# Kernel optimization log

Hardware: AMD Instinct MI355X
Metric: run time of the kernel (lower is better)

Reference implementation:

```python
import jax, jax.numpy as jnp
import numpy as np

NUM_GRAPHS = 64
N, E, H = 100000, 3200000, 64


def _glorot(k, shape):
    fan_in = shape[0]
    return jax.random.normal(k, shape, jnp.float32) * (1.0 / np.sqrt(fan_in))


def setup_inputs() -> dict:
    key = jax.random.key(0)
    ks = jax.random.split(key, 16)
    edge_index = jax.random.randint(ks[0], (2, E), 0, N)
    edge_weight = jax.random.uniform(ks[1], (E,), dtype=jnp.float32)
    batch = jnp.sort(jax.random.randint(ks[2], (N,), 0, NUM_GRAPHS))
    return {
        "edge_index": edge_index,
        "edge_weight": edge_weight,
        "batch": batch,
        "num_nodes": N,
        "W1": _glorot(ks[3], (1, H)), "b1": jnp.zeros((H,), jnp.float32),
        "W2": _glorot(ks[4], (H, H)), "b2": jnp.zeros((H,), jnp.float32),
        "W3": _glorot(ks[5], (H, H)), "b3": jnp.zeros((H,), jnp.float32),
        "W4": _glorot(ks[6], (H, H)), "b4": jnp.zeros((H,), jnp.float32),
        "W5": _glorot(ks[7], (H, H)), "b5": jnp.zeros((H,), jnp.float32),
        "lin_w": _glorot(ks[8], (H, 1)), "lin_b": jnp.zeros((1,), jnp.float32),
    }


def _gcn_layer(x, W, b, src, dst, w, n):
    # GCNConv(normalize=False): linear transform then weighted scatter-add over edges.
    h = x @ W                                  # [N, H]
    m = h[src] * w[:, None]                    # [E, H] messages
    return jax.ops.segment_sum(m, dst, num_segments=n) + b


def reference(edge_index, edge_weight, batch, num_nodes,
              W1, b1, W2, b2, W3, b3, W4, b4, W5, b5, lin_w, lin_b):
    src, dst = edge_index[0], edge_index[1]
    x = jnp.ones((num_nodes, 1), jnp.float32)
    for W, b in ((W1, b1), (W2, b2), (W3, b3), (W4, b4), (W5, b5)):
        x = jax.nn.relu(_gcn_layer(x, W, b, src, dst, edge_weight, num_nodes))
        # dropout p=0.1 is identity in eval mode
    # global mean pool per graph
    sums = jax.ops.segment_sum(x, batch, num_segments=NUM_GRAPHS)      # [G, H]
    counts = jax.ops.segment_sum(jnp.ones((num_nodes,), x.dtype), batch,
                                 num_segments=NUM_GRAPHS)
    pooled = sums / jnp.maximum(counts, 1.0)[:, None]
    return pooled @ lin_w + lin_b                                      # [G, 1]
```

## Files before the change

### kernel.cpp

```cpp
#include <hip/hip_runtime.h>

#define H 64
#define NUM_GRAPHS 64
#define BSHIFT 8
#define BSIZE 256
#define MAXNB 512
#define CHUNK 8192
#define BKT 9216
#define PADE 8
#define CSRB (BKT + BSIZE * PADE)
#define RPB 16

typedef unsigned int uint;
typedef unsigned short ushort;
typedef __attribute__((ext_vector_type(4))) float f32x4;
typedef __attribute__((ext_vector_type(8))) short short8;

__device__ __forceinline__ float bf2f(ushort u) {
    return __uint_as_float(((uint)u) << 16);
}
__device__ __forceinline__ ushort f2bf(float f) {
    uint b = __float_as_uint(f);
    b += 0x7FFFu + ((b >> 16) & 1u);
    return (ushort)(b >> 16);
}

__global__ void init_kernel(int* __restrict__ bucketCur, int NB) {
    int i = blockIdx.x * 256 + threadIdx.x;
    if (i < NB) bucketCur[i] = i * BKT;
}

__global__ __launch_bounds__(1024) void part_kernel(const int* __restrict__ src,
        const int* __restrict__ dst, const float* __restrict__ w,
        int* __restrict__ bucketCur, int2* __restrict__ bucketed, int E, int NB) {
    __shared__ int h[MAXNB];
    __shared__ int basev[MAXNB];
    __shared__ int lbase[MAXNB + 1];
    __shared__ int s[512];
    __shared__ int2 stage[CHUNK];
    int tid = threadIdx.x;
    for (int i = tid; i < NB; i += 1024) h[i] = 0;
    __syncthreads();
    int cbase = blockIdx.x * CHUNK;
    int cend = min(cbase + CHUNK, E);
    for (int e = cbase + tid; e < cend; e += 1024)
        atomicAdd(&h[dst[e] >> BSHIFT], 1);
    __syncthreads();
    for (int i = tid; i < NB; i += 1024) {
        int c = h[i];
        basev[i] = c ? atomicAdd(&bucketCur[i], c) : 0;
    }
    if (tid < 512) s[tid] = (tid < NB) ? h[tid] : 0;
    __syncthreads();
    for (int off = 1; off < 512; off <<= 1) {
        int t = (tid < 512 && tid >= off) ? s[tid - off] : 0;
        __syncthreads();
        if (tid < 512) s[tid] += t;
        __syncthreads();
    }
    if (tid < NB) lbase[tid + 1] = s[tid];
    if (tid == 0) lbase[0] = 0;
    __syncthreads();
    for (int i = tid; i < NB; i += 1024) h[i] = 0;
    __syncthreads();
    for (int e = cbase + tid; e < cend; e += 1024) {
        int d = dst[e];
        int b = d >> BSHIFT;
        int slot = atomicAdd(&h[b], 1);
        stage[lbase[b] + slot] =
            make_int2(((d & (BSIZE - 1)) << 17) | src[e], __float_as_int(w[e]));
    }
    __syncthreads();
    int lane = tid & 63, wv = tid >> 6;
    for (int b = wv; b < NB; b += 16) {
        int lb = lbase[b], cnt = lbase[b + 1] - lb, gb = basev[b];
        int lim = (b + 1) * BKT;
        for (int k = lane; k < cnt; k += 64)
            if (gb + k < lim) bucketed[gb + k] = stage[lb + k];
    }
}

__global__ __launch_bounds__(512) void bsort_kernel(const int* __restrict__ bucketCur,
        const int2* __restrict__ bucketed, uint* __restrict__ csr,
        int2* __restrict__ rowinfo, float* __restrict__ degw, int N) {
    __shared__ int cnt[BSIZE];
    __shared__ int pos[BSIZE];
    __shared__ int cur[BSIZE];
    __shared__ float wsum[BSIZE];
    int b = blockIdx.x;
    int tid = threadIdx.x;
    int nodeBase = b << BSHIFT;
    int nNodes = min(BSIZE, N - nodeBase);
    if (tid < BSIZE) { cnt[tid] = 0; wsum[tid] = 0.f; }
    __syncthreads();
    int ebeg = b * BKT;
    int eend = min(bucketCur[b], ebeg + BKT);
    for (int e = ebeg + tid; e < eend; e += 512)
        atomicAdd(&cnt[bucketed[e].x >> 17], 1);
    __syncthreads();
    int pc = 0;
    if (tid < BSIZE) { pc = (cnt[tid] + PADE - 1) & ~(PADE - 1); pos[tid] = pc; }
    __syncthreads();
    for (int off = 1; off < BSIZE; off <<= 1) {
        int t = (tid < BSIZE && tid >= off) ? pos[tid - off] : 0;
        __syncthreads();
        if (tid < BSIZE) pos[tid] += t;
        __syncthreads();
    }
    int csrBase = b * CSRB;
    if (tid < BSIZE) {
        int excl = pos[tid] - pc;
        cur[tid] = excl;
        if (tid < nNodes) rowinfo[nodeBase + tid] = make_int2(csrBase + excl, cnt[tid]);
    }
    __syncthreads();
    for (int e = ebeg + tid; e < eend; e += 512) {
        int2 v = bucketed[e];
        int dl = v.x >> 17;
        int slot = atomicAdd(&cur[dl], 1);
        uint wb = (uint)v.y;
        wb += 0x7FFFu + ((wb >> 16) & 1u);
        uint w15 = (wb >> 16) & 0x7FFFu;
        csr[csrBase + slot] = (((uint)(v.x & 0x1FFFF)) << 15) | w15;
        atomicAdd(&wsum[dl], __uint_as_float(w15 << 16));
    }
    __syncthreads();
    if (tid < nNodes) degw[nodeBase + tid] = wsum[tid];
}

__global__ void layer1_kernel(const float* __restrict__ degw, const float* __restrict__ W1,
                              const float* __restrict__ b1, ushort* __restrict__ out, int N) {
    int gid = blockIdx.x * 256 + threadIdx.x;
    if (gid >= N * 16) return;
    int i = gid >> 4, c4 = (gid & 15) * 4;
    float d = degw[i];
    uint lo = (uint)f2bf(fmaxf(d * W1[c4 + 0] + b1[c4 + 0], 0.f))
            | ((uint)f2bf(fmaxf(d * W1[c4 + 1] + b1[c4 + 1], 0.f)) << 16);
    uint hi = (uint)f2bf(fmaxf(d * W1[c4 + 2] + b1[c4 + 2], 0.f))
            | ((uint)f2bf(fmaxf(d * W1[c4 + 3] + b1[c4 + 3], 0.f)) << 16);
    *reinterpret_cast<uint2*>(out + ((size_t)i << 6) + c4) = make_uint2(lo, hi);
}

__global__ void count_kernel(const int* __restrict__ batch, float* __restrict__ gcnt, int N) {
    __shared__ int bins[NUM_GRAPHS];
    int tid = threadIdx.x;
    if (tid < NUM_GRAPHS) bins[tid] = 0;
    __syncthreads();
    int node = blockIdx.x * 256 + tid;
    if (node < N) atomicAdd(&bins[batch[node]], 1);
    __syncthreads();
    if (tid < NUM_GRAPHS && bins[tid])
        unsafeAtomicAdd(&gcnt[tid], (float)bins[tid]);
}

template<bool LAST>
__global__ __launch_bounds__(256) void layer_kernel(const int2* __restrict__ rowinfo,
        const uint* __restrict__ csr, const ushort* __restrict__ x,
        const float* __restrict__ W, const float* __restrict__ bvec,
        ushort* __restrict__ out, const int* __restrict__ batch,
        const float* __restrict__ linw, float* __restrict__ gsum, int N) {
    __shared__ alignas(16) ushort Wt[64][72];
    __shared__ alignas(16) ushort AG[RPB][72];
    __shared__ uint pc[4][64];
    __shared__ float gbins[NUM_GRAPHS];
    int tid = threadIdx.x;
    for (int i = tid; i < 64 * 64; i += 256) {
        int k = i >> 6, c = i & 63;
        Wt[c][k] = f2bf(W[i]);
    }
    if (LAST && tid < NUM_GRAPHS) gbins[tid] = 0.f;
    __syncthreads();
    int lane = tid & 63, wid = tid >> 6;
    int hi = lane >> 5;
    const char* xb = (const char*)x + (size_t)((lane & 31) << 2);
    int rowbase = blockIdx.x * RPB;
#pragma unroll 1
    for (int p = 0; p < 4; ++p) {
        int trow = wid * 4 + p;
        int row = rowbase + trow;
        float a0 = 0.f, a1 = 0.f, b0 = 0.f, b1 = 0.f;
        if (row < N) {
            int2 ri = rowinfo[row];
            int beg = ri.x, len = ri.y;
#pragma unroll 1
            for (int ck = 0; ck < len; ck += 64) {
                int idx = ck + lane;
                uint pv = (idx < len) ? __builtin_nontemporal_load(csr + beg + idx) : 0u;
                pc[wid][lane] = pv;
                int grps = (min(64, len - ck) + 7) >> 3;
#pragma unroll
                for (int g = 0; g < 8; ++g) {
                    if (g < grps) {
#pragma unroll
                        for (int jp = 0; jp < 4; ++jp) {
                            uint pp = pc[wid][g * 8 + jp * 2 + hi];
                            uint u = *reinterpret_cast<const uint*>(
                                         xb + ((size_t)(pp >> 15) << 7));
                            float wf = __uint_as_float((pp & 0x7FFFu) << 16);
                            if (g & 1) {
                                b0 = fmaf(wf, __uint_as_float(u << 16), b0);
                                b1 = fmaf(wf, __uint_as_float(u & 0xFFFF0000u), b1);
                            } else {
                                a0 = fmaf(wf, __uint_as_float(u << 16), a0);
                                a1 = fmaf(wf, __uint_as_float(u & 0xFFFF0000u), a1);
                            }
                        }
                    }
                }
            }
        }
        a0 += b0; a1 += b1;
        a0 += __shfl_xor(a0, 32);
        a1 += __shfl_xor(a1, 32);
        if (lane < 32) {
            uint pk = (uint)f2bf(a0) | ((uint)f2bf(a1) << 16);
            *reinterpret_cast<uint*>(&AG[trow][lane << 1]) = pk;
        }
    }
    __syncthreads();
    int cl = lane & 15, kg = lane >> 4;
    int c0 = wid * 16;
    short8 a0v = *reinterpret_cast<const short8*>(&AG[cl][kg * 8]);
    short8 a1v = *reinterpret_cast<const short8*>(&AG[cl][32 + kg * 8]);
    short8 bb0 = *reinterpret_cast<const short8*>(&Wt[c0 + cl][kg * 8]);
    short8 bb1 = *reinterpret_cast<const short8*>(&Wt[c0 + cl][32 + kg * 8]);
    f32x4 acc = {0.f, 0.f, 0.f, 0.f};
    acc = __builtin_amdgcn_mfma_f32_16x16x32_bf16(a0v, bb0, acc, 0, 0, 0);
    acc = __builtin_amdgcn_mfma_f32_16x16x32_bf16(a1v, bb1, acc, 0, 0, 0);
    float bias = bvec[c0 + cl];
    float lw = LAST ? linw[c0 + cl] : 0.f;
#pragma unroll
    for (int j = 0; j < 4; ++j) {
        int r = rowbase + kg * 4 + j;
        if (r < N) {
            float v = fmaxf(acc[j] + bias, 0.f);
            if (!LAST)
                __builtin_nontemporal_store(f2bf(v), out + ((size_t)r << 6) + c0 + cl);
            else
                atomicAdd(&gbins[batch[r]], v * lw);
        }
    }
    if (LAST) {
        __syncthreads();
        if (tid < NUM_GRAPHS) unsafeAtomicAdd(&gsum[tid], gbins[tid]);
    }
}

__global__ void final_kernel(const float* __restrict__ gsum, const float* __restrict__ gcnt,
                             const float* __restrict__ lin_b, float* __restrict__ out) {
    int g = threadIdx.x;
    if (g < NUM_GRAPHS) out[g] = gsum[g] / fmaxf(gcnt[g], 1.f) + lin_b[0];
}

extern "C" void kernel_launch(void* const* d_in, const int* in_sizes, int n_in,
                              void* d_out, int out_size, void* d_ws, size_t ws_size,
                              hipStream_t stream) {
    const int*   edge_index = (const int*)d_in[0];
    const float* ew    = (const float*)d_in[1];
    const int*   batch = (const int*)d_in[2];
    const float* W1    = (const float*)d_in[4];
    const float* b1    = (const float*)d_in[5];
    const float* Wl[4] = {(const float*)d_in[6], (const float*)d_in[8],
                          (const float*)d_in[10], (const float*)d_in[12]};
    const float* bl[4] = {(const float*)d_in[7], (const float*)d_in[9],
                          (const float*)d_in[11], (const float*)d_in[13]};
    const float* linw  = (const float*)d_in[14];
    const float* linb  = (const float*)d_in[15];

    const int E = in_sizes[1];
    const int N = in_sizes[2];
    const int* src = edge_index;
    const int* dst = edge_index + E;
    const int NB = (N + BSIZE - 1) >> BSHIFT;

    char* base = (char*)d_ws;
    size_t featPad = (((size_t)(N + 16) * H * 2) + 255) & ~(size_t)255;
    size_t bktBytes = (((size_t)NB * BKT * 8) + 255) & ~(size_t)255;
    size_t span = 2 * featPad > bktBytes ? 2 * featPad : bktBytes;
    ushort* bufA = (ushort*)base;
    ushort* bufB = (ushort*)(base + featPad);
    int2* bucketed = (int2*)base;
    uint* csr = (uint*)(base + span);
    size_t csrBytes = (((size_t)NB * CSRB * 4) + 255) & ~(size_t)255;
    char* tail = base + span + csrBytes;
    int2* rowinfo   = (int2*)tail;
    int* bucketCur  = (int*)(rowinfo + N);
    float* gsum     = (float*)(bucketCur + MAXNB);
    float* gcnt     = gsum + NUM_GRAPHS;
    float* degw     = gcnt + NUM_GRAPHS;

    const int chunks = (E + CHUNK - 1) / CHUNK;

    init_kernel<<<(NB + 255) / 256, 256, 0, stream>>>(bucketCur, NB);
    hipMemsetAsync(gsum, 0, 2 * NUM_GRAPHS * sizeof(float), stream);
    part_kernel<<<chunks, 1024, 0, stream>>>(src, dst, ew, bucketCur, bucketed, E, NB);
    bsort_kernel<<<NB, 512, 0, stream>>>(bucketCur, bucketed, csr, rowinfo, degw, N);

    layer1_kernel<<<(N * 16 + 255) / 256, 256, 0, stream>>>(degw, W1, b1, bufA, N);
    count_kernel<<<(N + 255) / 256, 256, 0, stream>>>(batch, gcnt, N);

    const int gridL = (N + RPB - 1) / RPB;
    ushort* xin = bufA;
    ushort* xout = bufB;
    for (int l = 0; l < 3; ++l) {
        layer_kernel<false><<<gridL, 256, 0, stream>>>(rowinfo, csr, xin, Wl[l], bl[l],
                xout, batch, linw, gsum, N);
        ushort* t = xin; xin = xout; xout = t;
    }
    layer_kernel<true><<<gridL, 256, 0, stream>>>(rowinfo, csr, xin, Wl[3], bl[3],
            xout, batch, linw, gsum, N);

    final_kernel<<<1, 64, 0, stream>>>(gsum, gcnt, linb, (float*)d_out);
}
```

Baseline: 470.0 us.

## Split GCN layers into column-sliced aggregation and separate MFMA transform kernels

Features are stored as two 32-column bf16 slices instead of row-major 64-wide rows. Each layer is split into an aggregation kernel and a matmul kernel. The aggregation kernel gathers from one slice, with block ids interleaved so neighbouring chunks share a slice. The matmul kernel applies W, bias and ReLU with MFMA over several row tiles per block. The aim is a smaller gather working set per pass so it stays in cache better, at the cost of two launches per layer, an extra round trip of the aggregate through memory, and reading the CSR twice.

```diff
diff --git a/kernel.cpp b/kernel.cpp
--- a/kernel.cpp
+++ b/kernel.cpp
@@ -9,7 +9,6 @@
 #define BKT 9216
 #define PADE 8
 #define CSRB (BKT + BSIZE * PADE)
-#define RPB 16
 
 typedef unsigned int uint;
 typedef unsigned short ushort;
@@ -129,7 +128,7 @@
 }
 
 __global__ void layer1_kernel(const float* __restrict__ degw, const float* __restrict__ W1,
-                              const float* __restrict__ b1, ushort* __restrict__ out, int N) {
+                              const float* __restrict__ b1, ushort* __restrict__ outB, int N) {
     int gid = blockIdx.x * 256 + threadIdx.x;
     if (gid >= N * 16) return;
     int i = gid >> 4, c4 = (gid & 15) * 4;
@@ -138,7 +137,8 @@
             | ((uint)f2bf(fmaxf(d * W1[c4 + 1] + b1[c4 + 1], 0.f)) << 16);
     uint hi = (uint)f2bf(fmaxf(d * W1[c4 + 2] + b1[c4 + 2], 0.f))
             | ((uint)f2bf(fmaxf(d * W1[c4 + 3] + b1[c4 + 3], 0.f)) << 16);
-    *reinterpret_cast<uint2*>(out + ((size_t)i << 6) + c4) = make_uint2(lo, hi);
+    size_t off = (size_t)(c4 >> 5) * N * 32 + ((size_t)i << 5) + (c4 & 31);
+    *reinterpret_cast<uint2*>(outB + off) = make_uint2(lo, hi);
 }
 
 __global__ void count_kernel(const int* __restrict__ batch, float* __restrict__ gcnt, int N) {
@@ -153,15 +153,62 @@
         unsafeAtomicAdd(&gcnt[tid], (float)bins[tid]);
 }
 
-template<bool LAST>
-__global__ __launch_bounds__(256) void layer_kernel(const int2* __restrict__ rowinfo,
-        const uint* __restrict__ csr, const ushort* __restrict__ x,
+__global__ __launch_bounds__(256) void aggA_kernel(const int2* __restrict__ rowinfo,
+        const uint* __restrict__ csr, const ushort* __restrict__ xB,
+        ushort* __restrict__ aggB, int N, int nchunk) {
+    __shared__ uint pc[4][64];
+    int b = blockIdx.x;
+    int r8 = b & 7;
+    int slice = r8 >> 2;
+    int chunk = (b >> 3) * 4 + (r8 & 3);
+    if (chunk >= nchunk) return;
+    int rowbase = chunk * 16;
+    int tid = threadIdx.x, lane = tid & 63, wid = tid >> 6;
+    int hi = lane >> 5;
+    int lch = lane & 31;
+    const char* xsb = (const char*)(xB + (size_t)slice * N * 32) + (lch << 1);
+    ushort* asb = aggB + (size_t)slice * N * 32 + lch;
+    int pcb = hi << 5;
+#pragma unroll 1
+    for (int p = 0; p < 2; ++p) {
+        int row = rowbase + wid * 4 + p * 2 + hi;
+        int rr = min(row, N - 1);
+        int2 ri = rowinfo[rr];
+        int beg = ri.x;
+        int len = (row < N) ? ri.y : 0;
+        int lenm = max(len, __shfl_xor(len, 32));
+        float a0 = 0.f, a1 = 0.f;
+#pragma unroll 1
+        for (int ck = 0; ck < lenm; ck += 32) {
+            int idx = ck + lch;
+            uint pv = (idx < len) ? __builtin_nontemporal_load(csr + beg + idx) : 0u;
+            pc[wid][pcb + lch] = pv;
+            int rem = len - ck;
+#pragma unroll
+            for (int g = 0; g < 4; ++g) {
+                if (g * 8 < rem) {
+#pragma unroll
+                    for (int j = 0; j < 8; ++j) {
+                        uint pp = pc[wid][pcb + g * 8 + j];
+                        float wf = __uint_as_float((pp & 0x7FFFu) << 16);
+                        ushort u = *reinterpret_cast<const ushort*>(
+                                       xsb + ((size_t)(pp >> 15) << 6));
+                        if (g & 1) a1 = fmaf(wf, bf2f(u), a1);
+                        else       a0 = fmaf(wf, bf2f(u), a0);
+                    }
+                }
+            }
+        }
+        if (row < N) asb[(size_t)row << 5] = f2bf(a0 + a1);
+    }
+}
+
+template<bool LAST, int TILES>
+__global__ __launch_bounds__(256) void matB_kernel(const ushort* __restrict__ aggB,
         const float* __restrict__ W, const float* __restrict__ bvec,
-        ushort* __restrict__ out, const int* __restrict__ batch,
+        ushort* __restrict__ outB, const int* __restrict__ batch,
         const float* __restrict__ linw, float* __restrict__ gsum, int N) {
     __shared__ alignas(16) ushort Wt[64][72];
-    __shared__ alignas(16) ushort AG[RPB][72];
-    __shared__ uint pc[4][64];
     __shared__ float gbins[NUM_GRAPHS];
     int tid = threadIdx.x;
     for (int i = tid; i < 64 * 64; i += 256) {
@@ -171,73 +218,34 @@
     if (LAST && tid < NUM_GRAPHS) gbins[tid] = 0.f;
     __syncthreads();
     int lane = tid & 63, wid = tid >> 6;
-    int hi = lane >> 5;
-    const char* xb = (const char*)x + (size_t)((lane & 31) << 2);
-    int rowbase = blockIdx.x * RPB;
-#pragma unroll 1
-    for (int p = 0; p < 4; ++p) {
-        int trow = wid * 4 + p;
-        int row = rowbase + trow;
-        float a0 = 0.f, a1 = 0.f, b0 = 0.f, b1 = 0.f;
-        if (row < N) {
-            int2 ri = rowinfo[row];
-            int beg = ri.x, len = ri.y;
-#pragma unroll 1
-            for (int ck = 0; ck < len; ck += 64) {
-                int idx = ck + lane;
-                uint pv = (idx < len) ? __builtin_nontemporal_load(csr + beg + idx) : 0u;
-                pc[wid][lane] = pv;
-                int grps = (min(64, len - ck) + 7) >> 3;
-#pragma unroll
-                for (int g = 0; g < 8; ++g) {
-                    if (g < grps) {
-#pragma unroll
-                        for (int jp = 0; jp < 4; ++jp) {
-                            uint pp = pc[wid][g * 8 + jp * 2 + hi];
-                            uint u = *reinterpret_cast<const uint*>(
-                                         xb + ((size_t)(pp >> 15) << 7));
-                            float wf = __uint_as_float((pp & 0x7FFFu) << 16);
-                            if (g & 1) {
-                                b0 = fmaf(wf, __uint_as_float(u << 16), b0);
-                                b1 = fmaf(wf, __uint_as_float(u & 0xFFFF0000u), b1);
-                            } else {
-                                a0 = fmaf(wf, __uint_as_float(u << 16), a0);
-                                a1 = fmaf(wf, __uint_as_float(u & 0xFFFF0000u), a1);
-                            }
-                        }
-                    }
-                }
-            }
-        }
-        a0 += b0; a1 += b1;
-        a0 += __shfl_xor(a0, 32);
-        a1 += __shfl_xor(a1, 32);
-        if (lane < 32) {
-            uint pk = (uint)f2bf(a0) | ((uint)f2bf(a1) << 16);
-            *reinterpret_cast<uint*>(&AG[trow][lane << 1]) = pk;
-        }
-    }
-    __syncthreads();
     int cl = lane & 15, kg = lane >> 4;
     int c0 = wid * 16;
-    short8 a0v = *reinterpret_cast<const short8*>(&AG[cl][kg * 8]);
-    short8 a1v = *reinterpret_cast<const short8*>(&AG[cl][32 + kg * 8]);
-    short8 bb0 = *reinterpret_cast<const short8*>(&Wt[c0 + cl][kg * 8]);
-    short8 bb1 = *reinterpret_cast<const short8*>(&Wt[c0 + cl][32 + kg * 8]);
-    f32x4 acc = {0.f, 0.f, 0.f, 0.f};
-    acc = __builtin_amdgcn_mfma_f32_16x16x32_bf16(a0v, bb0, acc, 0, 0, 0);
-    acc = __builtin_amdgcn_mfma_f32_16x16x32_bf16(a1v, bb1, acc, 0, 0, 0);
-    float bias = bvec[c0 + cl];
-    float lw = LAST ? linw[c0 + cl] : 0.f;
+    int cc = c0 + cl;
+    size_t oblk = (size_t)(cc >> 5) * N * 32;
+    for (int t = 0; t < TILES; ++t) {
+        int rowbase = (blockIdx.x * TILES + t) * 16;
+        if (rowbase >= N) break;
+        const ushort* ap0 = aggB + (((size_t)(rowbase + cl)) << 5) + kg * 8;
+        short8 a0v = *reinterpret_cast<const short8*>(ap0);
+        short8 a1v = *reinterpret_cast<const short8*>(ap0 + (size_t)N * 32);
+        short8 bb0 = *reinterpret_cast<const short8*>(&Wt[cc][kg * 8]);
+        short8 bb1 = *reinterpret_cast<const short8*>(&Wt[cc][32 + kg * 8]);
+        f32x4 acc = {0.f, 0.f, 0.f, 0.f};
+        acc = __builtin_amdgcn_mfma_f32_16x16x32_bf16(a0v, bb0, acc, 0, 0, 0);
+        acc = __builtin_amdgcn_mfma_f32_16x16x32_bf16(a1v, bb1, acc, 0, 0, 0);
+        float bias = bvec[cc];
+        float lw = LAST ? linw[cc] : 0.f;
 #pragma unroll
-    for (int j = 0; j < 4; ++j) {
-        int r = rowbase + kg * 4 + j;
-        if (r < N) {
-            float v = fmaxf(acc[j] + bias, 0.f);
-            if (!LAST)
-                __builtin_nontemporal_store(f2bf(v), out + ((size_t)r << 6) + c0 + cl);
-            else
-                atomicAdd(&gbins[batch[r]], v * lw);
+        for (int j = 0; j < 4; ++j) {
+            int r = rowbase + kg * 4 + j;
+            if (r < N) {
+                float v = fmaxf(acc[j] + bias, 0.f);
+                if (!LAST)
+                    __builtin_nontemporal_store(f2bf(v),
+                        outB + oblk + ((size_t)r << 5) + (cc & 31));
+                else
+                    atomicAdd(&gbins[batch[r]], v * lw);
+            }
         }
     }
     if (LAST) {
@@ -276,9 +284,10 @@
     char* base = (char*)d_ws;
     size_t featPad = (((size_t)(N + 16) * H * 2) + 255) & ~(size_t)255;
     size_t bktBytes = (((size_t)NB * BKT * 8) + 255) & ~(size_t)255;
-    size_t span = 2 * featPad > bktBytes ? 2 * featPad : bktBytes;
+    size_t span = 3 * featPad > bktBytes ? 3 * featPad : bktBytes;
     ushort* bufA = (ushort*)base;
     ushort* bufB = (ushort*)(base + featPad);
+    ushort* bufC = (ushort*)(base + 2 * featPad);
     int2* bucketed = (int2*)base;
     uint* csr = (uint*)(base + span);
     size_t csrBytes = (((size_t)NB * CSRB * 4) + 255) & ~(size_t)255;
@@ -299,15 +308,19 @@
     layer1_kernel<<<(N * 16 + 255) / 256, 256, 0, stream>>>(degw, W1, b1, bufA, N);
     count_kernel<<<(N + 255) / 256, 256, 0, stream>>>(batch, gcnt, N);
 
-    const int gridL = (N + RPB - 1) / RPB;
+    const int nchunk = (N + 15) / 16;
+    const int gridA = 8 * ((nchunk + 3) / 4);
+    const int nt16 = (N + 15) / 16;
     ushort* xin = bufA;
     ushort* xout = bufB;
     for (int l = 0; l < 3; ++l) {
-        layer_kernel<false><<<gridL, 256, 0, stream>>>(rowinfo, csr, xin, Wl[l], bl[l],
+        aggA_kernel<<<gridA, 256, 0, stream>>>(rowinfo, csr, xin, bufC, N, nchunk);
+        matB_kernel<false, 2><<<(nt16 + 1) / 2, 256, 0, stream>>>(bufC, Wl[l], bl[l],
                 xout, batch, linw, gsum, N);
         ushort* t = xin; xin = xout; xout = t;
     }
-    layer_kernel<true><<<gridL, 256, 0, stream>>>(rowinfo, csr, xin, Wl[3], bl[3],
+    aggA_kernel<<<gridA, 256, 0, stream>>>(rowinfo, csr, xin, bufC, N, nchunk);
+    matB_kernel<true, 8><<<(nt16 + 7) / 8, 256, 0, stream>>>(bufC, Wl[3], bl[3],
             xout, batch, linw, gsum, N);
 
     final_kernel<<<1, 64, 0, stream>>>(gsum, gcnt, linb, (float*)d_out);
```

After: 470.2 us. No clear change (+0.0%).
